# Kernel optimization log

Measured on AMD Instinct MI355X. Metric: run time of the kernel, lower is better.

The kernel has to match this reference:

```python
import jax, jax.numpy as jnp
import numpy as np

NUM_BINS = 24


def setup_inputs() -> dict:
    key = jax.random.key(0)
    k1, k2 = jax.random.split(key)
    x = jax.random.normal(k1, (64, 1, 512, 512), dtype=jnp.float32)
    y = jax.random.normal(k2, (64, 1, 512, 512), dtype=jnp.float32)
    return {"x": x, "y": y}


def reference(x, y):
    nb = NUM_BINS
    B = x.shape[0]
    # torch.no_grad() downsample -> stop_gradient
    xs = jax.lax.stop_gradient(x[:, :, ::2, ::2])
    ys = jax.lax.stop_gradient(y[:, :, ::2, ::2])
    # small additive noise (randn_like * 1e-4), fixed key for determinism
    nk1, nk2 = jax.random.split(jax.random.key(42))
    xs = xs + jax.random.normal(nk1, xs.shape, xs.dtype) * 0.0001
    ys = ys + jax.random.normal(nk2, ys.shape, ys.dtype) * 0.0001
    x_flat = xs.reshape(B, -1)
    y_flat = ys.reshape(B, -1)
    x_flat = jnp.clip((x_flat + 1.0) * 0.5, 0.001, 0.999)
    y_flat = jnp.clip((y_flat + 1.0) * 0.5, 0.001, 0.999)
    # bucketize against linspace(0,1,nb+1) minus 1 == floor(v*nb), clamped
    x_bin = jnp.clip(jnp.floor(x_flat * nb).astype(jnp.int32), 0, nb - 1)
    y_bin = jnp.clip(jnp.floor(y_flat * nb).astype(jnp.int32), 0, nb - 1)
    # joint histogram for all batches at once via one segment_sum
    batch_off = (jnp.arange(B, dtype=jnp.int32) * (nb * nb))[:, None]
    seg = (batch_off + x_bin * nb + y_bin).reshape(-1)
    ones = jnp.ones(seg.shape, dtype=jnp.float32)
    hist = jax.ops.segment_sum(ones, seg, num_segments=B * nb * nb)
    joint = hist.reshape(B, nb, nb)
    total = joint.sum(axis=(1, 2), keepdims=True) + 1e-10
    joint = joint / total  # [B, nb, nb]
    x_hist = joint.sum(axis=2)  # [B, nb]
    y_hist = joint.sum(axis=1)  # [B, nb]
    eps = 1e-05
    joint_e = joint + eps
    xh = x_hist + eps
    yh = y_hist + eps
    log_joint = jnp.log(joint_e)
    log_prod = jnp.log(xh[:, :, None] * yh[:, None, :])
    mi = jnp.sum(joint_e * (log_joint - log_prod), axis=(1, 2))  # [B]
    hx = -jnp.sum(xh * jnp.log(xh), axis=1)
    hy = -jnp.sum(yh * jnp.log(yh), axis=1)
    se = hx + hy
    nmi = jnp.where(se < 1e-10, 0.0, 2.0 * mi / se)
    nmi = jnp.clip(nmi, -1.0, 1.0)
    return -jnp.clip(jnp.mean(nmi), -1.0, 1.0)
```

## Files before the change

### kernel.cpp

```cpp
#include <hip/hip_runtime.h>
#include <stdint.h>
#include <stddef.h>


#define NB 24
#define NBINS 576
#define NBATCH 64
#define SPB 65536
#define HIST_BPB 16
#define HIST_THREADS 256

__host__ __device__ __forceinline__ uint32_t rotl32_(uint32_t x, uint32_t r) {
  return (x << r) | (x >> (32u - r));
}

__host__ __device__ inline void threefry2x32_(uint32_t k0, uint32_t k1,
                                              uint32_t& x0, uint32_t& x1) {
  const uint32_t k2 = k0 ^ k1 ^ 0x1BD11BDAu;
  x0 += k0; x1 += k1;
#define TFR(r) { x0 += x1; x1 = rotl32_(x1, (r)); x1 ^= x0; }
  TFR(13u) TFR(15u) TFR(26u) TFR(6u)
  x0 += k1; x1 += k2 + 1u;
  TFR(17u) TFR(29u) TFR(16u) TFR(24u)
  x0 += k2; x1 += k0 + 2u;
  TFR(13u) TFR(15u) TFR(26u) TFR(6u)
  x0 += k0; x1 += k1 + 3u;
  TFR(17u) TFR(29u) TFR(16u) TFR(24u)
  x0 += k1; x1 += k2 + 4u;
  TFR(13u) TFR(15u) TFR(26u) TFR(6u)
  x0 += k2; x1 += k0 + 5u;
#undef TFR
}

__device__ __forceinline__ float erfinv32_(float x) {
  float w = -log1pf(-x * x);
  float p;
  if (w < 5.0f) {
    w -= 2.5f;
    p =  2.81022636e-08f;
    p = fmaf(p, w,  3.43273939e-07f);
    p = fmaf(p, w, -3.5233877e-06f);
    p = fmaf(p, w, -4.39150654e-06f);
    p = fmaf(p, w,  0.00021858087f);
    p = fmaf(p, w, -0.00125372503f);
    p = fmaf(p, w, -0.00417768164f);
    p = fmaf(p, w,  0.246640727f);
    p = fmaf(p, w,  1.50140941f);
  } else {
    w = sqrtf(w) - 3.0f;
    p = -0.000200214257f;
    p = fmaf(p, w,  0.000100950558f);
    p = fmaf(p, w,  0.00134934322f);
    p = fmaf(p, w, -0.00367342844f);
    p = fmaf(p, w,  0.00573950773f);
    p = fmaf(p, w, -0.0076224613f);
    p = fmaf(p, w,  0.00943887047f);
    p = fmaf(p, w,  1.00167406f);
    p = fmaf(p, w,  2.83297682f);
  }
  return p * x;
}

__device__ __forceinline__ float tf_normal_(uint32_t ka, uint32_t kb, uint32_t n) {
  uint32_t x0 = 0u, x1 = n;
  threefry2x32_(ka, kb, x0, x1);
  const uint32_t bits = x0 ^ x1;
  float f = __uint_as_float((bits >> 9) | 0x3F800000u) - 1.0f;
  const float lo = -0.99999994f;
  float u = f * 2.0f + lo;
  u = fmaxf(lo, u);
  return 1.41421356f * erfinv32_(u);
}

__global__ __launch_bounds__(HIST_THREADS) void nmi_hist_kernel(
    const float* __restrict__ x, const float* __restrict__ y,
    uint32_t* __restrict__ ghist,
    uint32_t nk1a, uint32_t nk1b, uint32_t nk2a, uint32_t nk2b) {
  __shared__ uint32_t h[NBINS];
  for (int t = threadIdx.x; t < NBINS; t += HIST_THREADS) h[t] = 0u;
  __syncthreads();

  const int b    = blockIdx.x / HIST_BPB;
  const int blk  = blockIdx.x % HIST_BPB;
  const int per  = SPB / HIST_BPB;
  const int base = blk * per;
  const float* __restrict__ xb = x + (size_t)b * 262144;
  const float* __restrict__ yb = y + (size_t)b * 262144;
  const uint32_t nbase = (uint32_t)b * (uint32_t)SPB;

  for (int i = threadIdx.x; i < per; i += HIST_THREADS) {
    const int s  = base + i;
    const int hh = s >> 8;
    const int ww = s & 255;
    const int src = (hh << 10) + (ww << 1);
    float xv = xb[src];
    float yv = yb[src];
    const uint32_t n = nbase + (uint32_t)s;
    xv = xv + tf_normal_(nk1a, nk1b, n) * 1e-4f;
    yv = yv + tf_normal_(nk2a, nk2b, n) * 1e-4f;
    float vx = (xv + 1.0f) * 0.5f;
    float vy = (yv + 1.0f) * 0.5f;
    vx = fminf(fmaxf(vx, 0.001f), 0.999f);
    vy = fminf(fmaxf(vy, 0.001f), 0.999f);
    int bx = (int)floorf(vx * 24.0f);
    int by = (int)floorf(vy * 24.0f);
    bx = bx < 0 ? 0 : (bx > 23 ? 23 : bx);
    by = by < 0 ? 0 : (by > 23 ? 23 : by);
    atomicAdd(&h[bx * NB + by], 1u);
  }
  __syncthreads();

  uint32_t* gh = ghist + b * NBINS;
  for (int t = threadIdx.x; t < NBINS; t += HIST_THREADS) {
    const uint32_t c = h[t];
    if (c) atomicAdd(&gh[t], c);
  }
}

__global__ __launch_bounds__(256) void nmi_reduce_kernel(
    const uint32_t* __restrict__ ghist, float* __restrict__ nmi_out) {
  const int b = blockIdx.x;
  __shared__ float joint[NBINS];
  __shared__ float xh[NB];
  __shared__ float yh[NB];
  __shared__ float red_mi[4];
  __shared__ float red_h[4];

  const uint32_t* gh = ghist + b * NBINS;
  for (int t = threadIdx.x; t < NBINS; t += 256)
    joint[t] = (float)gh[t] * (1.0f / 65536.0f);
  __syncthreads();

  if (threadIdx.x < NB) {
    const int i = threadIdx.x;
    float sx = 0.f, sy = 0.f;
    for (int j = 0; j < NB; ++j) {
      sx += joint[i * NB + j];
      sy += joint[j * NB + i];
    }
    xh[i] = sx; yh[i] = sy;
  }
  __syncthreads();

  float mi_part = 0.f;
  for (int t = threadIdx.x; t < NBINS; t += 256) {
    const int i = t / NB, j = t % NB;
    const float je = joint[t] + 1e-5f;
    const float pe = (xh[i] + 1e-5f) * (yh[j] + 1e-5f);
    mi_part += je * (logf(je) - logf(pe));
  }
  float h_part = 0.f;
  if (threadIdx.x < NB) {
    const float e = xh[threadIdx.x] + 1e-5f;
    h_part = -(e * logf(e));
  } else if (threadIdx.x >= 64 && threadIdx.x < 64 + NB) {
    const float e = yh[threadIdx.x - 64] + 1e-5f;
    h_part = -(e * logf(e));
  }

  for (int o = 32; o > 0; o >>= 1) {
    mi_part += __shfl_down(mi_part, o);
    h_part  += __shfl_down(h_part, o);
  }
  const int wid  = threadIdx.x >> 6;
  const int lane = threadIdx.x & 63;
  if (lane == 0) { red_mi[wid] = mi_part; red_h[wid] = h_part; }
  __syncthreads();
  if (threadIdx.x == 0) {
    const float mi = red_mi[0] + red_mi[1] + red_mi[2] + red_mi[3];
    const float se = red_h[0] + red_h[1] + red_h[2] + red_h[3];
    float nmi = (se < 1e-10f) ? 0.0f : (2.0f * mi / se);
    nmi = fminf(fmaxf(nmi, -1.0f), 1.0f);
    nmi_out[b] = nmi;
  }
}

__global__ void nmi_final_kernel(const float* __restrict__ nmi,
                                 float* __restrict__ out) {
  float v = nmi[threadIdx.x];
  for (int o = 32; o > 0; o >>= 1) v += __shfl_down(v, o);
  if (threadIdx.x == 0) {
    float m = v * (1.0f / 64.0f);
    m = fminf(fmaxf(m, -1.0f), 1.0f);
    out[0] = -m;
  }
}

extern "C" void kernel_launch(void* const* d_in, const int* in_sizes, int n_in,
                              void* d_out, int out_size, void* d_ws, size_t ws_size,
                              hipStream_t stream) {
  const float* x = (const float*)d_in[0];
  const float* y = (const float*)d_in[1];
  float* out = (float*)d_out;

  uint32_t* ghist = (uint32_t*)d_ws;
  float* nmi = (float*)((char*)d_ws + (size_t)NBATCH * NBINS * sizeof(uint32_t));

  uint32_t nk1a = 0u, nk1b = 0u; threefry2x32_(0u, 42u, nk1a, nk1b);
  uint32_t nk2a = 0u, nk2b = 1u; threefry2x32_(0u, 42u, nk2a, nk2b);

  hipMemsetAsync(ghist, 0, (size_t)NBATCH * NBINS * sizeof(uint32_t), stream);
  nmi_hist_kernel<<<NBATCH * HIST_BPB, HIST_THREADS, 0, stream>>>(
      x, y, ghist, nk1a, nk1b, nk2a, nk2b);
  nmi_reduce_kernel<<<NBATCH, 256, 0, stream>>>(ghist, nmi);
  nmi_final_kernel<<<1, 64, 0, stream>>>(nmi, out);
}
```

Before: 165.9 us.

## Skip RNG noise for samples far from bin edges; fuse final reduction

Samples whose scaled value sits more than a small margin from a bin boundary are binned directly, without running the Threefry RNG and erfinv. Noise of magnitude about 1e-4 cannot move such samples across a boundary. Near-edge samples go into a shared-memory queue and are processed with the exact noisy path in a second pass, or inline if the queue overflows. The final mean kernel is folded into the reduce kernel through a last-block atomic counter, and the histogram block size is doubled to 512 threads. The margin is exact only if the noise never exceeds the bound; extreme normal draws could in principle cross it.

```diff
diff --git a/kernel.cpp b/kernel.cpp
--- a/kernel.cpp
+++ b/kernel.cpp
@@ -8,7 +8,10 @@
 #define NBATCH 64
 #define SPB 65536
 #define HIST_BPB 16
-#define HIST_THREADS 256
+#define HIST_THREADS 512
+#define PER_BLOCK 4096
+#define QCAP 1024
+#define MARGIN 0.008f
 
 __host__ __device__ __forceinline__ uint32_t rotl32_(uint32_t x, uint32_t r) {
   return (x << r) | (x >> (32u - r));
@@ -77,31 +80,64 @@
     uint32_t* __restrict__ ghist,
     uint32_t nk1a, uint32_t nk1b, uint32_t nk2a, uint32_t nk2b) {
   __shared__ uint32_t h[NBINS];
+  __shared__ uint16_t q[QCAP];
+  __shared__ uint32_t qn;
   for (int t = threadIdx.x; t < NBINS; t += HIST_THREADS) h[t] = 0u;
+  if (threadIdx.x == 0) qn = 0u;
   __syncthreads();
 
   const int b    = blockIdx.x / HIST_BPB;
   const int blk  = blockIdx.x % HIST_BPB;
-  const int per  = SPB / HIST_BPB;
-  const int base = blk * per;
+  const int base = blk * PER_BLOCK;
   const float* __restrict__ xb = x + (size_t)b * 262144;
   const float* __restrict__ yb = y + (size_t)b * 262144;
   const uint32_t nbase = (uint32_t)b * (uint32_t)SPB;
 
-  for (int i = threadIdx.x; i < per; i += HIST_THREADS) {
-    const int s  = base + i;
-    const int hh = s >> 8;
-    const int ww = s & 255;
-    const int src = (hh << 10) + (ww << 1);
-    float xv = xb[src];
-    float yv = yb[src];
+  #pragma unroll
+  for (int k = 0; k < PER_BLOCK / HIST_THREADS; ++k) {
+    const int i = k * HIST_THREADS + (int)threadIdx.x;
+    const int s = base + i;
+    const int src = ((s >> 8) << 10) + ((s & 255) << 1);
+    const float xv = xb[src];
+    const float yv = yb[src];
+    const float tx = fminf(fmaxf((xv + 1.0f) * 0.5f, 0.001f), 0.999f) * 24.0f;
+    const float ty = fminf(fmaxf((yv + 1.0f) * 0.5f, 0.001f), 0.999f) * 24.0f;
+    const float fx = floorf(tx), fy = floorf(ty);
+    const float rx = tx - fx,   ry = ty - fy;
+    const bool safe = (rx >= MARGIN) & (rx <= 1.0f - MARGIN) &
+                      (ry >= MARGIN) & (ry <= 1.0f - MARGIN);
+    if (safe) {
+      atomicAdd(&h[(int)fx * NB + (int)fy], 1u);
+    } else {
+      const uint32_t qi = atomicAdd(&qn, 1u);
+      if (qi < QCAP) {
+        q[qi] = (uint16_t)i;
+      } else {
+        const uint32_t n = nbase + (uint32_t)s;
+        const float xn = xv + tf_normal_(nk1a, nk1b, n) * 1e-4f;
+        const float yn = yv + tf_normal_(nk2a, nk2b, n) * 1e-4f;
+        const float vx = fminf(fmaxf((xn + 1.0f) * 0.5f, 0.001f), 0.999f);
+        const float vy = fminf(fmaxf((yn + 1.0f) * 0.5f, 0.001f), 0.999f);
+        int bx = (int)floorf(vx * 24.0f);
+        int by = (int)floorf(vy * 24.0f);
+        bx = bx < 0 ? 0 : (bx > 23 ? 23 : bx);
+        by = by < 0 ? 0 : (by > 23 ? 23 : by);
+        atomicAdd(&h[bx * NB + by], 1u);
+      }
+    }
+  }
+  __syncthreads();
+
+  const uint32_t nq = qn < QCAP ? qn : (uint32_t)QCAP;
+  for (uint32_t j = threadIdx.x; j < nq; j += HIST_THREADS) {
+    const int i = (int)q[j];
+    const int s = base + i;
+    const int src = ((s >> 8) << 10) + ((s & 255) << 1);
     const uint32_t n = nbase + (uint32_t)s;
-    xv = xv + tf_normal_(nk1a, nk1b, n) * 1e-4f;
-    yv = yv + tf_normal_(nk2a, nk2b, n) * 1e-4f;
-    float vx = (xv + 1.0f) * 0.5f;
-    float vy = (yv + 1.0f) * 0.5f;
-    vx = fminf(fmaxf(vx, 0.001f), 0.999f);
-    vy = fminf(fmaxf(vy, 0.001f), 0.999f);
+    const float xn = xb[src] + tf_normal_(nk1a, nk1b, n) * 1e-4f;
+    const float yn = yb[src] + tf_normal_(nk2a, nk2b, n) * 1e-4f;
+    const float vx = fminf(fmaxf((xn + 1.0f) * 0.5f, 0.001f), 0.999f);
+    const float vy = fminf(fmaxf((yn + 1.0f) * 0.5f, 0.001f), 0.999f);
     int bx = (int)floorf(vx * 24.0f);
     int by = (int)floorf(vy * 24.0f);
     bx = bx < 0 ? 0 : (bx > 23 ? 23 : bx);
@@ -118,13 +154,15 @@
 }
 
 __global__ __launch_bounds__(256) void nmi_reduce_kernel(
-    const uint32_t* __restrict__ ghist, float* __restrict__ nmi_out) {
+    const uint32_t* __restrict__ ghist, float* __restrict__ nmi_arr,
+    uint32_t* __restrict__ ctr, float* __restrict__ out) {
   const int b = blockIdx.x;
   __shared__ float joint[NBINS];
   __shared__ float xh[NB];
   __shared__ float yh[NB];
   __shared__ float red_mi[4];
   __shared__ float red_h[4];
+  __shared__ int islast;
 
   const uint32_t* gh = ghist + b * NBINS;
   for (int t = threadIdx.x; t < NBINS; t += 256)
@@ -166,23 +204,29 @@
   const int lane = threadIdx.x & 63;
   if (lane == 0) { red_mi[wid] = mi_part; red_h[wid] = h_part; }
   __syncthreads();
+
   if (threadIdx.x == 0) {
     const float mi = red_mi[0] + red_mi[1] + red_mi[2] + red_mi[3];
     const float se = red_h[0] + red_h[1] + red_h[2] + red_h[3];
     float nmi = (se < 1e-10f) ? 0.0f : (2.0f * mi / se);
     nmi = fminf(fmaxf(nmi, -1.0f), 1.0f);
-    nmi_out[b] = nmi;
-  }
-}
-
-__global__ void nmi_final_kernel(const float* __restrict__ nmi,
-                                 float* __restrict__ out) {
-  float v = nmi[threadIdx.x];
-  for (int o = 32; o > 0; o >>= 1) v += __shfl_down(v, o);
-  if (threadIdx.x == 0) {
-    float m = v * (1.0f / 64.0f);
-    m = fminf(fmaxf(m, -1.0f), 1.0f);
-    out[0] = -m;
+    __hip_atomic_store(&nmi_arr[b], nmi, __ATOMIC_RELEASE,
+                       __HIP_MEMORY_SCOPE_AGENT);
+    const uint32_t t = __hip_atomic_fetch_add(ctr, 1u, __ATOMIC_ACQ_REL,
+                                              __HIP_MEMORY_SCOPE_AGENT);
+    islast = (t == (uint32_t)(NBATCH - 1));
+  }
+  __syncthreads();
+
+  if (islast && threadIdx.x < 64) {
+    float v = __hip_atomic_load(&nmi_arr[threadIdx.x], __ATOMIC_ACQUIRE,
+                                __HIP_MEMORY_SCOPE_AGENT);
+    for (int o = 32; o > 0; o >>= 1) v += __shfl_down(v, o);
+    if (threadIdx.x == 0) {
+      float m = v * (1.0f / 64.0f);
+      m = fminf(fmaxf(m, -1.0f), 1.0f);
+      out[0] = -m;
+    }
   }
 }
 
@@ -194,14 +238,14 @@
   float* out = (float*)d_out;
 
   uint32_t* ghist = (uint32_t*)d_ws;
-  float* nmi = (float*)((char*)d_ws + (size_t)NBATCH * NBINS * sizeof(uint32_t));
+  uint32_t* ctr   = (uint32_t*)((char*)d_ws + 147456);
+  float*    nmi   = (float*)((char*)d_ws + 147520);
 
   uint32_t nk1a = 0u, nk1b = 0u; threefry2x32_(0u, 42u, nk1a, nk1b);
   uint32_t nk2a = 0u, nk2b = 1u; threefry2x32_(0u, 42u, nk2a, nk2b);
 
-  hipMemsetAsync(ghist, 0, (size_t)NBATCH * NBINS * sizeof(uint32_t), stream);
+  hipMemsetAsync(d_ws, 0, 147520 + NBATCH * sizeof(float), stream);
   nmi_hist_kernel<<<NBATCH * HIST_BPB, HIST_THREADS, 0, stream>>>(
       x, y, ghist, nk1a, nk1b, nk2a, nk2b);
-  nmi_reduce_kernel<<<NBATCH, 256, 0, stream>>>(ghist, nmi);
-  nmi_final_kernel<<<1, 64, 0, stream>>>(nmi, out);
-}
+  nmi_reduce_kernel<<<NBATCH, 256, 0, stream>>>(ghist, nmi, ctr, out);
+}
```

Measured after the change: 138.2 us. -16.7%, faster.
